# Kernel tuning notes

Hardware: AMD Instinct MI355X
Metric: run time of the kernel (lower is better)

## Reference

```python
import jax, jax.numpy as jnp
import numpy as np

B, S_ENC, S_DEC = 4, 2048, 1024
ENC_DIM, DEC_DIM, H = 1024, 1024, 16
CROSS_DIM = max(ENC_DIM, DEC_DIM)
HEAD_DIM_DEC = DEC_DIM // H
SCALE = HEAD_DIM_DEC ** 0.5  # module divides by dec_scaling only


def _linear_params(key, d_in, d_out):
    kw, kb = jax.random.split(key)
    bound = 1.0 / np.sqrt(d_in)
    W = jax.random.uniform(kw, (d_in, d_out), jnp.float32, -bound, bound)
    b = jax.random.uniform(kb, (d_out,), jnp.float32, -bound, bound)
    return W, b


def setup_inputs() -> dict:
    key = jax.random.key(0)
    ks = jax.random.split(key, 7)
    enc = jax.random.normal(ks[0], (B, S_ENC, ENC_DIM), jnp.float32)
    dec = jax.random.normal(ks[1], (B, S_DEC, DEC_DIM), jnp.float32)
    enc_mask = jax.random.uniform(ks[2], (B, 1, 1, S_ENC)) < 0.1
    q_w, q_b = _linear_params(ks[3], DEC_DIM, CROSS_DIM)
    k_w, k_b = _linear_params(ks[4], ENC_DIM, CROSS_DIM)
    v_w, v_b = _linear_params(ks[5], ENC_DIM, DEC_DIM)
    o_w, o_b = _linear_params(ks[6], DEC_DIM, DEC_DIM)
    return {"enc": enc, "enc_mask": enc_mask, "dec": dec,
            "q_w": q_w, "q_b": q_b, "k_w": k_w, "k_b": k_b,
            "v_w": v_w, "v_b": v_b, "o_w": o_w, "o_b": o_b}


def _split_heads(x):
    b, s, d = x.shape
    return x.reshape(b, s, H, d // H).transpose(0, 2, 1, 3)  # [b,h,s,hd]


def reference(enc, enc_mask, dec, q_w, q_b, k_w, k_b, v_w, v_b, o_w, o_b):
    q = _split_heads(dec @ q_w + q_b)   # [B,H,Sq,cross_hd]
    k = _split_heads(enc @ k_w + k_b)   # [B,H,Sk,cross_hd]
    v = _split_heads(enc @ v_w + v_b)   # [B,H,Sk,dec_hd]
    logits = jnp.einsum('bhqd,bhkd->bhqk', q, k) / SCALE
    logits = jnp.where(enc_mask, -jnp.inf, logits)
    a = jax.nn.softmax(logits, axis=-1)
    x = jnp.einsum('bhqk,bhkd->bhqd', a, v)          # [B,H,Sq,dec_hd]
    x = x.transpose(0, 2, 1, 3).reshape(x.shape[0], x.shape[2], -1)  # [B,Sq,DEC_DIM]
    return x @ o_w + o_b
```

## Files before the change

### kernel.cpp

```cpp
#include <hip/hip_runtime.h>
#include <hip/hip_bf16.h>
#include <cstdint>

#define BB   4
#define SENC 2048
#define SDEC 1024
#define DM   1024
#define NH   16
#define HD   64

using short8 = __attribute__((ext_vector_type(8))) short;
using f32x4  = __attribute__((ext_vector_type(4))) float;

__device__ inline unsigned short f2bf(float f) {
    return (unsigned short)((__builtin_bit_cast(unsigned int, f) + 0x8000u) >> 16);
}
__device__ inline unsigned int pk2bf(float a, float b) {
    return ((__builtin_bit_cast(unsigned int, a) + 0x8000u) >> 16) |
           ((__builtin_bit_cast(unsigned int, b) + 0x8000u) & 0xffff0000u);
}

__device__ inline float fexp2(float x) {
#if __has_builtin(__builtin_amdgcn_exp2f)
    return __builtin_amdgcn_exp2f(x);
#else
    return exp2f(x);
#endif
}

#if __has_builtin(__builtin_amdgcn_global_load_lds)
#define HAS_GLL 1
#endif

__device__ inline void stage16(const void* g, void* l) {
#ifdef HAS_GLL
    typedef __attribute__((address_space(1))) const unsigned int guint;
    typedef __attribute__((address_space(3))) unsigned int luint;
    __builtin_amdgcn_global_load_lds((guint*)g, (luint*)l, 16, 0, 0);
#else
    *(short8*)l = *(const short8*)g;
#endif
}

__global__ __launch_bounds__(256) void prep_kernel(
    const float* __restrict__ dec, const float* __restrict__ enc,
    unsigned short* __restrict__ actb,
    const float* __restrict__ qw, const float* __restrict__ kw,
    const float* __restrict__ vw, const float* __restrict__ ow,
    unsigned short* __restrict__ qwt, unsigned short* __restrict__ kvwt,
    unsigned short* __restrict__ owt) {
    __shared__ float t[64][65];
    const int id = blockIdx.x, tid = threadIdx.x;
    if (id < 12288) {
        const int nd = BB * SDEC * DM;
        int i = (id * 256 + tid) * 4;
        const float* src = (i < nd) ? (dec + i) : (enc + (i - nd));
        float4 v = *(const float4*)src;
        ushort4 o;
        o.x = f2bf(v.x); o.y = f2bf(v.y); o.z = f2bf(v.z); o.w = f2bf(v.w);
        *(ushort4*)(actb + i) = o;
        return;
    }
    const int id2 = id - 12288;
    const int z = id2 >> 8, ky = (id2 >> 4) & 15, nx = id2 & 15;
    const float* src; unsigned short* dst;
    switch (z) {
        case 0:  src = qw; dst = qwt; break;
        case 1:  src = kw; dst = kvwt; break;
        case 2:  src = vw; dst = kvwt + (size_t)64 * 16384; break;
        default: src = ow; dst = owt; break;
    }
    const int k0 = ky * 64, n0 = nx * 64;
    #pragma unroll
    for (int it = 0; it < 16; ++it) {
        int e = it * 256 + tid, r = e >> 6, c = e & 63;
        t[r][c] = src[(size_t)(k0 + r) * DM + n0 + c];
    }
    __syncthreads();
    #pragma unroll
    for (int it = 0; it < 16; ++it) {
        int e = it * 256 + tid, r = e >> 6, c = e & 63;
        size_t off = (size_t)((n0 + r) >> 4) * 16384 + (size_t)((k0 + c) >> 3) * 128
                   + ((r & 15) << 3) + (c & 7);
        dst[off] = f2bf(t[c][r]);
    }
}

__global__ __launch_bounds__(256) void gemm_qkv_kernel(
    const unsigned short* __restrict__ encb, const unsigned short* __restrict__ decb,
    const unsigned short* __restrict__ kvwt, const unsigned short* __restrict__ qwt,
    const float* __restrict__ q_b, const float* __restrict__ k_b, const float* __restrict__ v_b,
    unsigned short* __restrict__ Qb, unsigned short* __restrict__ Kb,
    unsigned short* __restrict__ Vtb) {
    __shared__ __align__(16) unsigned short As[2][128 * 32];
    const int id = blockIdx.x;
    const bool isKV = id < 1024;
    const unsigned short *A, *Bw;
    int m0, n0;
    if (isKV) {
        const int x = id & 7, w = id >> 3;
        A = encb; Bw = kvwt;
        m0 = (x * 8 + (w >> 4)) * 128;
        n0 = (w & 15) * 128;
    } else {
        const int i2 = id - 1024, x = i2 & 7, w = i2 >> 3;
        A = decb; Bw = qwt;
        m0 = (x * 4 + (w >> 3)) * 128;
        n0 = (w & 7) * 128;
    }
    const int tid = threadIdx.x;
    const int wave = tid >> 6, lane = tid & 63, quad = lane >> 4, l16 = lane & 15;
    const int wr = wave >> 1, wc = wave & 1;
    const int r16 = lane >> 2, c8 = (lane & 3) * 8;
    f32x4 acc[4][4] = {};

    const unsigned short* Bbase = Bw + (size_t)(n0 >> 4) * 16384 + (size_t)(wc * 4) * 16384
                                + quad * 128 + l16 * 8;
    short8 bcur[4], bnxt[4];
    #pragma unroll
    for (int j = 0; j < 4; ++j) bcur[j] = *(const short8*)&Bbase[j * 16384];

    #pragma unroll
    for (int i = 0; i < 2; ++i) {
        const int row = wave * 32 + i * 16 + r16;
        stage16(&A[(size_t)(m0 + row) * DM + c8], &As[0][row * 32 + c8]);
    }
    for (int it = 0; it < 32; ++it) {
        const int bf = it & 1;
        __syncthreads();
        if (it < 31) {
            const int kb2 = (it + 1) * 32, nb = bf ^ 1;
            #pragma unroll
            for (int i = 0; i < 2; ++i) {
                const int row = wave * 32 + i * 16 + r16;
                stage16(&A[(size_t)(m0 + row) * DM + kb2 + c8], &As[nb][row * 32 + c8]);
            }
            #pragma unroll
            for (int j = 0; j < 4; ++j)
                bnxt[j] = *(const short8*)&Bbase[j * 16384 + kb2 * 16];
        }
        short8 af[4];
        #pragma unroll
        for (int i = 0; i < 4; ++i) af[i] = *(const short8*)&As[bf][(wr * 64 + i * 16 + l16) * 32 + quad * 8];
        #pragma unroll
        for (int i = 0; i < 4; ++i)
            #pragma unroll
            for (int j = 0; j < 4; ++j)
                acc[i][j] = __builtin_amdgcn_mfma_f32_16x16x32_bf16(af[i], bcur[j], acc[i][j], 0, 0, 0);
        #pragma unroll
        for (int j = 0; j < 4; ++j) bcur[j] = bnxt[j];
    }
    #pragma unroll
    for (int i = 0; i < 4; ++i) {
        #pragma unroll
        for (int j = 0; j < 4; ++j) {
            const int gc = n0 + wc * 64 + j * 16 + l16;
            const int gr0 = m0 + wr * 64 + i * 16 + quad * 4;
            if (!isKV) {
                const float bv = q_b[gc];
                const int h = gc >> 6, d = gc & 63;
                #pragma unroll
                for (int rr = 0; rr < 4; ++rr) {
                    int gr = gr0 + rr, b = gr >> 10, sq = gr & 1023;
                    float v = (acc[i][j][rr] + bv) * 0.18033688011112042f;
                    Qb[(((size_t)(b * NH + h) * SDEC + sq) << 6) + d] = f2bf(v);
                }
            } else if (gc < 1024) {
                const float bv = k_b[gc];
                const int h = gc >> 6, d = gc & 63;
                #pragma unroll
                for (int rr = 0; rr < 4; ++rr) {
                    int gr = gr0 + rr, b = gr >> 11, sk = gr & 2047;
                    size_t off = (size_t)(b * NH + h) * 131072 + (size_t)(sk >> 4) * 1024
                               + ((d >> 3) << 7) + ((sk & 15) << 3) + (d & 7);
                    Kb[off] = f2bf(acc[i][j][rr] + bv);
                }
            } else {
                const int gc2 = gc & 1023;
                const float bv = v_b[gc2];
                const int h = gc2 >> 6, d = gc2 & 63;
                const int b = gr0 >> 11, sk0 = gr0 & 2047;
                size_t off = (size_t)(b * NH + h) * 131072 + (size_t)(d >> 4) * 32768
                           + (size_t)(sk0 >> 3) * 128 + ((d & 15) << 3) + (sk0 & 7);
                uint2 pk;
                pk.x = pk2bf(acc[i][j][0] + bv, acc[i][j][1] + bv);
                pk.y = pk2bf(acc[i][j][2] + bv, acc[i][j][3] + bv);
                *(uint2*)&Vtb[off] = pk;
            }
        }
    }
}

__global__ __launch_bounds__(256) void gemm_o_kernel(const unsigned short* __restrict__ A,
                                                     const unsigned short* __restrict__ Bw,
                                                     const float* __restrict__ bias,
                                                     float* __restrict__ Cout) {
    __shared__ __align__(16) unsigned short As[2][64 * 32];
    const int id = blockIdx.x, x = id & 7, w = id >> 3;
    const int m0 = (x * 8 + (w >> 3)) * 64, n0 = (w & 7) * 128;
    const int tid = threadIdx.x;
    const int wave = tid >> 6, lane = tid & 63, quad = lane >> 4, l16 = lane & 15;
    const int r16 = lane >> 2, c8 = (lane & 3) * 8;
    f32x4 acc[4][2] = {};
    const unsigned short* Bbase = Bw + (size_t)((n0 >> 4) + wave * 2) * 16384 + quad * 128 + l16 * 8;
    short8 bcur[2], bnxt[2];
    #pragma unroll
    for (int j = 0; j < 2; ++j) bcur[j] = *(const short8*)&Bbase[j * 16384];
    {
        const int rowA = wave * 16 + r16;
        stage16(&A[(size_t)(m0 + rowA) * DM + c8], &As[0][rowA * 32 + c8]);
    }
    for (int it = 0; it < 32; ++it) {
        const int bf = it & 1;
        __syncthreads();
        if (it < 31) {
            const int kb2 = (it + 1) * 32, nb = bf ^ 1;
            const int rowA = wave * 16 + r16;
            stage16(&A[(size_t)(m0 + rowA) * DM + kb2 + c8], &As[nb][rowA * 32 + c8]);
            #pragma unroll
            for (int j = 0; j < 2; ++j) bnxt[j] = *(const short8*)&Bbase[j * 16384 + kb2 * 16];
        }
        short8 af[4];
        #pragma unroll
        for (int i = 0; i < 4; ++i) af[i] = *(const short8*)&As[bf][(i * 16 + l16) * 32 + quad * 8];
        #pragma unroll
        for (int i = 0; i < 4; ++i)
            #pragma unroll
            for (int j = 0; j < 2; ++j)
                acc[i][j] = __builtin_amdgcn_mfma_f32_16x16x32_bf16(af[i], bcur[j], acc[i][j], 0, 0, 0);
        #pragma unroll
        for (int j = 0; j < 2; ++j) bcur[j] = bnxt[j];
    }
    #pragma unroll
    for (int i = 0; i < 4; ++i)
        #pragma unroll
        for (int j = 0; j < 2; ++j) {
            const int gc = n0 + wave * 32 + j * 16 + l16;
            const float bv = bias[gc];
            #pragma unroll
            for (int rr = 0; rr < 4; ++rr) {
                const int gr = m0 + i * 16 + quad * 4 + rr;
                Cout[(size_t)gr * DM + gc] = acc[i][j][rr] + bv;
            }
        }
}

__global__ __launch_bounds__(256) void attn_kernel(const unsigned short* __restrict__ Qb,
                                                   const unsigned short* __restrict__ Kb,
                                                   const unsigned short* __restrict__ Vtb,
                                                   const int* __restrict__ mask,
                                                   unsigned short* __restrict__ Xb) {
    __shared__ __align__(16) unsigned short Ps[4][16 * 72];
    const int id = blockIdx.x, x = id & 7, r = id >> 3;
    const int bh = x * 8 + (r & 7), qt = r >> 3;
    const int b = bh >> 4, h = bh & 15;
    const int q0 = qt * 128;
    const int tid = threadIdx.x, wave = tid >> 6, lane = tid & 63;
    const int quad = lane >> 4, l16 = lane & 15;
    const int lo = quad * 128 + l16 * 8;

    const unsigned short* Kfp = Kb + (size_t)bh * 131072;
    const unsigned short* Vfp = Vtb + (size_t)bh * 131072;
    const int* mp = mask + (size_t)b * SENC;

    short8 qf[2][2];
    {
        const unsigned short* Qp = Qb + ((size_t)bh * SDEC + q0 + wave * 32) * HD;
        #pragma unroll
        for (int g = 0; g < 2; ++g) {
            qf[g][0] = *(const short8*)&Qp[(g * 16 + l16) * HD + quad * 8];
            qf[g][1] = *(const short8*)&Qp[(g * 16 + l16) * HD + 32 + quad * 8];
        }
    }

    float lsum[2] = {0.f, 0.f};
    f32x4 o[2][4] = {};

    for (int kb = 0; kb < SENC; kb += 64) {
        short8 kA0[4], kA1[4], vB0[4], vB1[4];
        const unsigned short* kt = Kfp + (size_t)(kb >> 4) * 1024 + lo;
        const unsigned short* vt = Vfp + (size_t)(kb >> 3) * 128 + lo;
        #pragma unroll
        for (int j = 0; j < 4; ++j) {
            kA0[j] = *(const short8*)&kt[j * 1024];
            kA1[j] = *(const short8*)&kt[j * 1024 + 512];
            vB0[j] = *(const short8*)&vt[j * 32768];
            vB1[j] = *(const short8*)&vt[j * 32768 + 512];
        }
        int4 mi[4];
        #pragma unroll
        for (int j = 0; j < 4; ++j) mi[j] = *(const int4*)&mp[kb + j * 16 + quad * 4];
        #pragma unroll
        for (int g = 0; g < 2; ++g) {
            f32x4 st[4];
            #pragma unroll
            for (int j = 0; j < 4; ++j) {
                f32x4 z = {0.f, 0.f, 0.f, 0.f};
                z = __builtin_amdgcn_mfma_f32_16x16x32_bf16(kA0[j], qf[g][0], z, 0, 0, 0);
                st[j] = __builtin_amdgcn_mfma_f32_16x16x32_bf16(kA1[j], qf[g][1], z, 0, 0, 0);
            }
            #pragma unroll
            for (int j = 0; j < 4; ++j) {
                float p0 = mi[j].x ? 0.f : fexp2(st[j][0]);
                float p1 = mi[j].y ? 0.f : fexp2(st[j][1]);
                float p2 = mi[j].z ? 0.f : fexp2(st[j][2]);
                float p3 = mi[j].w ? 0.f : fexp2(st[j][3]);
                lsum[g] += (p0 + p1) + (p2 + p3);
                uint2 pkv;
                pkv.x = pk2bf(p0, p1);
                pkv.y = pk2bf(p2, p3);
                *(uint2*)&Ps[wave][l16 * 72 + j * 16 + quad * 4] = pkv;
            }
            asm volatile("s_waitcnt lgkmcnt(0)" ::: "memory");
            short8 pA0 = *(const short8*)&Ps[wave][l16 * 72 + quad * 8];
            short8 pA1 = *(const short8*)&Ps[wave][l16 * 72 + 32 + quad * 8];
            #pragma unroll
            for (int dj = 0; dj < 4; ++dj) {
                o[g][dj] = __builtin_amdgcn_mfma_f32_16x16x32_bf16(pA0, vB0[dj], o[g][dj], 0, 0, 0);
                o[g][dj] = __builtin_amdgcn_mfma_f32_16x16x32_bf16(pA1, vB1[dj], o[g][dj], 0, 0, 0);
            }
        }
    }
    #pragma unroll
    for (int g = 0; g < 2; ++g) {
        float lg = lsum[g];
        lg += __shfl_xor(lg, 16);
        lg += __shfl_xor(lg, 32);
        #pragma unroll
        for (int rr = 0; rr < 4; ++rr) {
            float iv = 1.0f / __shfl(lg, quad * 4 + rr, 64);
            int sq = q0 + wave * 32 + g * 16 + quad * 4 + rr;
            #pragma unroll
            for (int dj = 0; dj < 4; ++dj)
                Xb[((size_t)(b * SDEC) + sq) * DM + h * HD + dj * 16 + l16] = f2bf(o[g][dj][rr] * iv);
        }
    }
}

extern "C" void kernel_launch(void* const* d_in, const int* in_sizes, int n_in,
                              void* d_out, int out_size, void* d_ws, size_t ws_size,
                              hipStream_t stream) {
    const float* enc   = (const float*)d_in[0];
    const int*   emask = (const int*)d_in[1];
    const float* dec   = (const float*)d_in[2];
    const float* q_w   = (const float*)d_in[3];
    const float* q_b   = (const float*)d_in[4];
    const float* k_w   = (const float*)d_in[5];
    const float* k_b   = (const float*)d_in[6];
    const float* v_w   = (const float*)d_in[7];
    const float* v_b   = (const float*)d_in[8];
    const float* o_w   = (const float*)d_in[9];
    const float* o_b   = (const float*)d_in[10];
    float* out = (float*)d_out;

    char* ws = (char*)d_ws;
    unsigned short* decb = (unsigned short*)ws; ws += (size_t)4096 * 1024 * 2;
    unsigned short* encb = (unsigned short*)ws; ws += (size_t)8192 * 1024 * 2;
    unsigned short* qwt  = (unsigned short*)ws; ws += (size_t)1024 * 1024 * 2;
    unsigned short* kvwt = (unsigned short*)ws; ws += (size_t)2048 * 1024 * 2;
    unsigned short* owt  = (unsigned short*)ws; ws += (size_t)1024 * 1024 * 2;
    unsigned short* Qb   = (unsigned short*)ws; ws += (size_t)BB * NH * SDEC * HD * 2;
    unsigned short* Kb   = (unsigned short*)ws; ws += (size_t)BB * NH * SENC * HD * 2;
    unsigned short* Vtb  = (unsigned short*)ws; ws += (size_t)BB * NH * HD * SENC * 2;
    unsigned short* Xb   = (unsigned short*)ws; ws += (size_t)4096 * 1024 * 2;

    prep_kernel<<<13312, 256, 0, stream>>>(dec, enc, decb, q_w, k_w, v_w, o_w, qwt, kvwt, owt);
    gemm_qkv_kernel<<<1280, 256, 0, stream>>>(encb, decb, kvwt, qwt, q_b, k_b, v_b, Qb, Kb, Vtb);
    attn_kernel<<<512, 256, 0, stream>>>(Qb, Kb, Vtb, emask, Xb);
    gemm_o_kernel<<<512, 256, 0, stream>>>(Xb, owt, o_b, out);
}
```

Measured before the change: 253.2 us.

## Restructure QKV GEMM into 256x128 tiles with swizzled LDS and ping-pong MFMA schedule

Rewrites the QKV projection GEMM to use 512-thread blocks computing 256x128 tiles with a 64-wide K step, halving the grid. The A tile is staged into a larger XOR-swizzled LDS buffer to avoid bank conflicts. The main loop uses explicit s_barrier, s_setprio and vmcnt waits to interleave LDS reads, global prefetch and MFMA bursts across waves. The aim is more data reuse per block and better overlap of memory traffic with matrix work. In exchange it uses more LDS and registers per block and relies on hand-placed waitcnt values that must match the issued load count.

```diff
diff --git a/kernel.cpp b/kernel.cpp
--- a/kernel.cpp
+++ b/kernel.cpp
@@ -86,70 +86,146 @@
     }
 }
 
-__global__ __launch_bounds__(256) void gemm_qkv_kernel(
+#define FENCE() asm volatile("" ::: "memory")
+#define BARRIER() do { FENCE(); __builtin_amdgcn_s_barrier(); FENCE(); } while (0)
+
+#define STAGE_TILE(kt, bufi) do { \
+    stage16(Ab + (kt) * 64,          &As[bufi][tid * 8]); \
+    stage16(Ab + 65536 + (kt) * 64,  &As[bufi][4096 + tid * 8]); \
+    stage16(Ab + 131072 + (kt) * 64, &As[bufi][8192 + tid * 8]); \
+    stage16(Ab + 196608 + (kt) * 64, &As[bufi][12288 + tid * 8]); \
+} while (0)
+
+#define LOADB(dst, kt) do { \
+    dst[0][0] = *(const short8*)&Bbase[(kt) * 1024]; \
+    dst[0][1] = *(const short8*)&Bbase[(kt) * 1024 + 512]; \
+    dst[1][0] = *(const short8*)&Bbase[16384 + (kt) * 1024]; \
+    dst[1][1] = *(const short8*)&Bbase[16384 + (kt) * 1024 + 512]; \
+    dst[2][0] = *(const short8*)&Bbase[32768 + (kt) * 1024]; \
+    dst[2][1] = *(const short8*)&Bbase[32768 + (kt) * 1024 + 512]; \
+    dst[3][0] = *(const short8*)&Bbase[49152 + (kt) * 1024]; \
+    dst[3][1] = *(const short8*)&Bbase[49152 + (kt) * 1024 + 512]; \
+} while (0)
+
+#define MFMA8(ii, a0, a1) do { \
+    acc[ii][0] = __builtin_amdgcn_mfma_f32_16x16x32_bf16(a0, bcur[0][0], acc[ii][0], 0, 0, 0); \
+    acc[ii][1] = __builtin_amdgcn_mfma_f32_16x16x32_bf16(a0, bcur[1][0], acc[ii][1], 0, 0, 0); \
+    acc[ii][2] = __builtin_amdgcn_mfma_f32_16x16x32_bf16(a0, bcur[2][0], acc[ii][2], 0, 0, 0); \
+    acc[ii][3] = __builtin_amdgcn_mfma_f32_16x16x32_bf16(a0, bcur[3][0], acc[ii][3], 0, 0, 0); \
+    acc[ii][0] = __builtin_amdgcn_mfma_f32_16x16x32_bf16(a1, bcur[0][1], acc[ii][0], 0, 0, 0); \
+    acc[ii][1] = __builtin_amdgcn_mfma_f32_16x16x32_bf16(a1, bcur[1][1], acc[ii][1], 0, 0, 0); \
+    acc[ii][2] = __builtin_amdgcn_mfma_f32_16x16x32_bf16(a1, bcur[2][1], acc[ii][2], 0, 0, 0); \
+    acc[ii][3] = __builtin_amdgcn_mfma_f32_16x16x32_bf16(a1, bcur[3][1], acc[ii][3], 0, 0, 0); \
+} while (0)
+
+__global__ __launch_bounds__(512, 2) void gemm_qkv_kernel(
     const unsigned short* __restrict__ encb, const unsigned short* __restrict__ decb,
     const unsigned short* __restrict__ kvwt, const unsigned short* __restrict__ qwt,
     const float* __restrict__ q_b, const float* __restrict__ k_b, const float* __restrict__ v_b,
     unsigned short* __restrict__ Qb, unsigned short* __restrict__ Kb,
     unsigned short* __restrict__ Vtb) {
-    __shared__ __align__(16) unsigned short As[2][128 * 32];
+    __shared__ __align__(16) unsigned short As[2][256 * 64];
     const int id = blockIdx.x;
-    const bool isKV = id < 1024;
+    const bool isKV = id < 512;
     const unsigned short *A, *Bw;
     int m0, n0;
     if (isKV) {
         const int x = id & 7, w = id >> 3;
         A = encb; Bw = kvwt;
-        m0 = (x * 8 + (w >> 4)) * 128;
+        m0 = (x * 4 + (w >> 4)) * 256;
         n0 = (w & 15) * 128;
     } else {
-        const int i2 = id - 1024, x = i2 & 7, w = i2 >> 3;
+        const int i2 = id - 512, x = i2 & 7, w = i2 >> 3;
         A = decb; Bw = qwt;
-        m0 = (x * 4 + (w >> 3)) * 128;
+        m0 = (x * 2 + (w >> 3)) * 256;
         n0 = (w & 7) * 128;
     }
     const int tid = threadIdx.x;
     const int wave = tid >> 6, lane = tid & 63, quad = lane >> 4, l16 = lane & 15;
     const int wr = wave >> 1, wc = wave & 1;
-    const int r16 = lane >> 2, c8 = (lane & 3) * 8;
     f32x4 acc[4][4] = {};
 
-    const unsigned short* Bbase = Bw + (size_t)(n0 >> 4) * 16384 + (size_t)(wc * 4) * 16384
-                                + quad * 128 + l16 * 8;
-    short8 bcur[4], bnxt[4];
-    #pragma unroll
-    for (int j = 0; j < 4; ++j) bcur[j] = *(const short8*)&Bbase[j * 16384];
-
-    #pragma unroll
-    for (int i = 0; i < 2; ++i) {
-        const int row = wave * 32 + i * 16 + r16;
-        stage16(&A[(size_t)(m0 + row) * DM + c8], &As[0][row * 32 + c8]);
-    }
-    for (int it = 0; it < 32; ++it) {
-        const int bf = it & 1;
-        __syncthreads();
-        if (it < 31) {
-            const int kb2 = (it + 1) * 32, nb = bf ^ 1;
-            #pragma unroll
-            for (int i = 0; i < 2; ++i) {
-                const int row = wave * 32 + i * 16 + r16;
-                stage16(&A[(size_t)(m0 + row) * DM + kb2 + c8], &As[nb][row * 32 + c8]);
-            }
-            #pragma unroll
-            for (int j = 0; j < 4; ++j)
-                bnxt[j] = *(const short8*)&Bbase[j * 16384 + kb2 * 16];
-        }
-        short8 af[4];
-        #pragma unroll
-        for (int i = 0; i < 4; ++i) af[i] = *(const short8*)&As[bf][(wr * 64 + i * 16 + l16) * 32 + quad * 8];
-        #pragma unroll
-        for (int i = 0; i < 4; ++i)
-            #pragma unroll
-            for (int j = 0; j < 4; ++j)
-                acc[i][j] = __builtin_amdgcn_mfma_f32_16x16x32_bf16(af[i], bcur[j], acc[i][j], 0, 0, 0);
-        #pragma unroll
-        for (int j = 0; j < 4; ++j) bcur[j] = bnxt[j];
-    }
+    const int srow = tid >> 3;
+    const int ksrc = ((tid ^ srow) & 7) * 8;
+    const unsigned short* Ab = A + (size_t)(m0 + srow) * 1024 + ksrc;
+
+    const unsigned short* Bbase = Bw + (size_t)((n0 >> 4) + wc * 4) * 16384 + quad * 128 + l16 * 8;
+    short8 bcur[4][2], bnxt[4][2];
+
+    const int rbase = (wr * 64 + l16) * 128;
+    const int rswz = (l16 & 7) << 4;
+    const int rk0 = (quad * 16) ^ rswz;
+    const int rk1 = (64 + quad * 16) ^ rswz;
+
+    STAGE_TILE(0, 0);
+    FENCE();
+    LOADB(bcur, 0);
+    FENCE();
+    STAGE_TILE(1, 1);
+    FENCE();
+    asm volatile("s_waitcnt vmcnt(12)" ::: "memory");
+    __builtin_amdgcn_s_barrier();
+    FENCE();
+
+    #pragma unroll
+    for (int kt = 0; kt <= 14; ++kt) {
+        const char* ap = (const char*)&As[kt & 1][0] + rbase;
+        short8 a00 = *(const short8*)(ap + rk0);
+        short8 a01 = *(const short8*)(ap + rk1);
+        short8 a10 = *(const short8*)(ap + 2048 + rk0);
+        short8 a11 = *(const short8*)(ap + 2048 + rk1);
+        if (kt >= 1) {
+            STAGE_TILE(kt + 1, (kt & 1) ^ 1);
+            FENCE();
+        }
+        LOADB(bnxt, kt + 1);
+        FENCE();
+        __builtin_amdgcn_s_barrier();
+        FENCE();
+        __builtin_amdgcn_s_setprio(1);
+        MFMA8(0, a00, a01);
+        MFMA8(1, a10, a11);
+        __builtin_amdgcn_s_setprio(0);
+        BARRIER();
+        short8 a20 = *(const short8*)(ap + 4096 + rk0);
+        short8 a21 = *(const short8*)(ap + 4096 + rk1);
+        short8 a30 = *(const short8*)(ap + 6144 + rk0);
+        short8 a31 = *(const short8*)(ap + 6144 + rk1);
+        FENCE();
+        __builtin_amdgcn_s_barrier();
+        FENCE();
+        __builtin_amdgcn_s_setprio(1);
+        MFMA8(2, a20, a21);
+        MFMA8(3, a30, a31);
+        __builtin_amdgcn_s_setprio(0);
+        asm volatile("s_waitcnt vmcnt(8)" ::: "memory");
+        __builtin_amdgcn_s_barrier();
+        FENCE();
+        bcur[0][0] = bnxt[0][0]; bcur[0][1] = bnxt[0][1];
+        bcur[1][0] = bnxt[1][0]; bcur[1][1] = bnxt[1][1];
+        bcur[2][0] = bnxt[2][0]; bcur[2][1] = bnxt[2][1];
+        bcur[3][0] = bnxt[3][0]; bcur[3][1] = bnxt[3][1];
+    }
+    {
+        const char* ap = (const char*)&As[1][0] + rbase;
+        short8 a00 = *(const short8*)(ap + rk0);
+        short8 a01 = *(const short8*)(ap + rk1);
+        short8 a10 = *(const short8*)(ap + 2048 + rk0);
+        short8 a11 = *(const short8*)(ap + 2048 + rk1);
+        __builtin_amdgcn_s_setprio(1);
+        MFMA8(0, a00, a01);
+        MFMA8(1, a10, a11);
+        __builtin_amdgcn_s_setprio(0);
+        short8 a20 = *(const short8*)(ap + 4096 + rk0);
+        short8 a21 = *(const short8*)(ap + 4096 + rk1);
+        short8 a30 = *(const short8*)(ap + 6144 + rk0);
+        short8 a31 = *(const short8*)(ap + 6144 + rk1);
+        __builtin_amdgcn_s_setprio(1);
+        MFMA8(2, a20, a21);
+        MFMA8(3, a30, a31);
+        __builtin_amdgcn_s_setprio(0);
+    }
+
     #pragma unroll
     for (int i = 0; i < 4; ++i) {
         #pragma unroll
@@ -365,7 +441,7 @@
     unsigned short* Xb   = (unsigned short*)ws; ws += (size_t)4096 * 1024 * 2;
 
     prep_kernel<<<13312, 256, 0, stream>>>(dec, enc, decb, q_w, k_w, v_w, o_w, qwt, kvwt, owt);
-    gemm_qkv_kernel<<<1280, 256, 0, stream>>>(encb, decb, kvwt, qwt, q_b, k_b, v_b, Qb, Kb, Vtb);
+    gemm_qkv_kernel<<<640, 512, 0, stream>>>(encb, decb, kvwt, qwt, q_b, k_b, v_b, Qb, Kb, Vtb);
     attn_kernel<<<512, 256, 0, stream>>>(Qb, Kb, Vtb, emask, Xb);
     gemm_o_kernel<<<512, 256, 0, stream>>>(Xb, owt, o_b, out);
 }
```

Measured after the change: 272.3 us. 7.5% more time.
